# Performance work log

Measured on AMD Instinct MI355X. Metric: run time of the kernel, lower is better.

## Reference

```python
import jax, jax.numpy as jnp
import numpy as np

B, V, N, C = 32, 5, 196, 768
H = 768          # hidden_dim of score MLP
NUM_ITERS = 3


def setup_inputs() -> dict:
    key = jax.random.key(0)
    ks = jax.random.split(key, 6)
    scale = 1.0 / np.sqrt(C)
    x = jax.random.normal(ks[0], (B, V, N, C), dtype=jnp.float32)
    # per-view projection weights, stacked: [V, C, C] (no bias)
    w_views = jax.random.uniform(ks[1], (V, C, C), dtype=jnp.float32, minval=-scale, maxval=scale)
    # score MLP: Linear(2C -> H), Tanh, Linear(H -> 1)
    s1 = 1.0 / np.sqrt(2 * C)
    w1 = jax.random.uniform(ks[2], (2 * C, H), dtype=jnp.float32, minval=-s1, maxval=s1)
    b1 = jax.random.uniform(ks[3], (H,), dtype=jnp.float32, minval=-s1, maxval=s1)
    s2 = 1.0 / np.sqrt(H)
    w2 = jax.random.uniform(ks[4], (H, 1), dtype=jnp.float32, minval=-s2, maxval=s2)
    b2 = jax.random.uniform(ks[5], (1,), dtype=jnp.float32, minval=-s2, maxval=s2)
    return {"x": x, "w_views": w_views, "w1": w1, "b1": b1, "w2": w2, "b2": b2}


def reference(x, w_views, w1, b1, w2, b2):
    # x: [B, V, N, C]
    c = x.mean(axis=1)                                   # [B, N, C]
    # per-view projections are independent of c: compute once (same math)
    proj_x = jnp.einsum('bvnc,vcd->bvnd', x, w_views)    # [B, V, N, C]
    a = None
    for _ in range(NUM_ITERS):
        c_exp = jnp.broadcast_to(c[:, None], x.shape)    # [B, V, N, C]
        si = jnp.concatenate([x, c_exp], axis=-1)        # [B, V, N, 2C]
        h = jnp.tanh(jnp.einsum('bvnk,kh->bvnh', si, w1) + b1)
        s = (jnp.einsum('bvnh,ho->bvno', h, w2) + b2)[..., 0]  # [B, V, N]
        a = jax.nn.softmax(s, axis=1)                    # softmax over views
        c = jnp.einsum('bvn,bvnc->bnc', a, proj_x)       # weighted sum over V
    eps = 1e-8
    entropy = -(a * jnp.log(a + eps)).sum(axis=1)        # [B, N]
    r = 1.0 - entropy / np.log(V)
    return c, r
```

## Files before the change

kernel.cpp:

```cpp
#include <hip/hip_runtime.h>

#define CDIM   768
#define NSEQ   196
#define NVIEW  5
#define BN_TOT 6272
#define SLAB   4816896
#define WSLAB  589824

typedef __attribute__((ext_vector_type(8))) short short8;
typedef __attribute__((ext_vector_type(4))) float f32x4;

__device__ __forceinline__ float bf_lo(unsigned u) { return __uint_as_float(u << 16); }
__device__ __forceinline__ float bf_hi(unsigned u) { return __uint_as_float(u & 0xffff0000u); }
__device__ __forceinline__ unsigned short f2bf(float f) {
  unsigned u = __float_as_uint(f);
  return (unsigned short)((u + 0x7fffu + ((u >> 16) & 1u)) >> 16);
}
__device__ __forceinline__ unsigned pack2(float f0, float f1) {
  return (unsigned)f2bf(f0) | ((unsigned)f2bf(f1) << 16);
}
__device__ __forceinline__ float ftanh(float x) {
  x = fminf(fmaxf(x, -10.f), 10.f);
  float e = __expf(2.f * x);
  return (e - 1.f) / (e + 1.f);
}
__device__ __forceinline__ void async_cp16(const void* g, void* l) {
  __builtin_amdgcn_global_load_lds((const __attribute__((address_space(1))) unsigned*)g,
                                   (__attribute__((address_space(3))) unsigned*)l, 16, 0, 0);
}

__global__ __launch_bounds__(256) void k_tr2(const float* __restrict__ wv,
                                             const float* __restrict__ w1,
                                             const float* __restrict__ x,
                                             unsigned short* __restrict__ wvT,
                                             unsigned short* __restrict__ w1aT,
                                             unsigned short* __restrict__ w1bT,
                                             unsigned short* __restrict__ wvB,
                                             unsigned short* __restrict__ cb) {
  const int m = blockIdx.z;
  const int tx = threadIdx.x, ty = threadIdx.y, t = ty * 32 + tx;
  if (m == 7) {
    const int bidx = blockIdx.y * 24 + blockIdx.x;
    if (t < 192) {
      const int col = t * 4;
      for (int i = 0; i < 11; ++i) {
        const int bn = bidx * 11 + i;
        if (bn >= BN_TOT) break;
        const int b = bn / NSEQ, n = bn - b * NSEQ;
        const float* xp = x + ((size_t)(b * NVIEW) * NSEQ + n) * CDIM + col;
        float s0 = 0, s1 = 0, s2 = 0, s3 = 0;
#pragma unroll
        for (int v = 0; v < NVIEW; ++v) {
          float4 p = *(const float4*)(xp + (size_t)v * (NSEQ * CDIM));
          s0 += p.x; s1 += p.y; s2 += p.z; s3 += p.w;
        }
        uint2 o;
        o.x = pack2(s0 * 0.2f, s1 * 0.2f);
        o.y = pack2(s2 * 0.2f, s3 * 0.2f);
        *(uint2*)(cb + (size_t)bn * CDIM + col) = o;
      }
    }
    return;
  }
  __shared__ float tile[32][33];
  const float* src;
  unsigned short* dst;
  unsigned short* dstB = nullptr;
  if (m < NVIEW)      { src = wv + (size_t)m * WSLAB; dst = wvT + (size_t)m * WSLAB;
                        dstB = wvB + (size_t)m * WSLAB; }
  else if (m == NVIEW){ src = w1;                     dst = w1aT; }
  else                { src = w1 + WSLAB;             dst = w1bT; }
  const int x0 = blockIdx.x * 32, y0 = blockIdx.y * 32;
#pragma unroll
  for (int i = 0; i < 4; ++i) {
    float v = src[(size_t)(y0 + ty + i * 8) * CDIM + x0 + tx];
    tile[ty + i * 8][tx] = v;
    if (dstB) dstB[(size_t)(y0 + ty + i * 8) * CDIM + x0 + tx] = f2bf(v);
  }
  __syncthreads();
#pragma unroll
  for (int i = 0; i < 4; ++i)
    dst[(size_t)(x0 + ty + i * 8) * CDIM + y0 + tx] = f2bf(tile[tx][ty + i * 8]);
}

__global__ __launch_bounds__(256, 4) void k_pre(const unsigned short* __restrict__ w1bT,
                                                const unsigned short* __restrict__ wvB,
                                                const unsigned short* __restrict__ cb,
                                                unsigned short* __restrict__ wpT,
                                                unsigned short* __restrict__ cw1) {
  __shared__ __align__(16) unsigned short lds[16384];
  const int wk = blockIdx.x;
  const int t = threadIdx.x, w = t >> 6, lane = t & 63, lr = lane & 15, lq = lane >> 4;
  const int wm = (w >> 1) * 64, wn = (w & 1) * 64;
  const unsigned short *Abf, *Bt;
  unsigned short* C;
  int mrow0, colBase;
  if (wk < 180) {
    const int v = wk / 36, rem = wk % 36;
    mrow0 = (rem / 6) * 128; colBase = (rem % 6) * 128;
    Abf = w1bT; Bt = wvB + (size_t)v * WSLAB; C = wpT + (size_t)v * WSLAB;
  } else {
    const int j = wk - 180;
    mrow0 = (j / 6) * 128; colBase = (j % 6) * 128;
    Abf = cb; Bt = w1bT; C = cw1;
  }
  const int swz = ((t & 3) ^ ((t >> 3) & 3)) << 3;
  const unsigned short* gA = Abf + (size_t)(mrow0 + (t >> 2)) * CDIM + swz;
  const unsigned short* gB = Bt + (size_t)(colBase + (t >> 2)) * CDIM + swz;
  const int kch = ((lq ^ ((lr >> 1) & 3)) << 3);
#define CPA(kt, s) { unsigned short* d_ = lds + (s) * 8192 + (w << 9);                  \
    async_cp16(gA + (kt) * 32, d_);                                                     \
    async_cp16(gA + (kt) * 32 + (size_t)64 * CDIM, d_ + 2048); }
#define CPB(kt, s) { unsigned short* d_ = lds + (s) * 8192 + 4096 + (w << 9);           \
    async_cp16(gB + (kt) * 32, d_);                                                     \
    async_cp16(gB + (kt) * 32 + (size_t)64 * CDIM, d_ + 2048); }
  f32x4 acc[4][4] = {};
  CPA(0, 0); CPB(0, 0);
  asm volatile("s_waitcnt vmcnt(0)" ::: "memory");
  __builtin_amdgcn_s_barrier();
  for (int kt = 0; kt < 24; ++kt) {
    const int s = kt & 1;
    const unsigned short* bp = lds + s * 8192;
    if (kt < 23) { CPA(kt + 1, s ^ 1); CPB(kt + 1, s ^ 1); }
    short8 af[4], bf[4];
#pragma unroll
    for (int i = 0; i < 4; ++i) af[i] = *(const short8*)(bp + (wm + i * 16 + lr) * 32 + kch);
#pragma unroll
    for (int j = 0; j < 4; ++j) bf[j] = *(const short8*)(bp + 4096 + (wn + j * 16 + lr) * 32 + kch);
    __builtin_amdgcn_s_setprio(1);
#pragma unroll
    for (int i = 0; i < 4; ++i)
#pragma unroll
      for (int j = 0; j < 4; ++j)
        acc[i][j] = __builtin_amdgcn_mfma_f32_16x16x32_bf16(af[i], bf[j], acc[i][j], 0, 0, 0);
    __builtin_amdgcn_s_setprio(0);
    asm volatile("s_waitcnt vmcnt(0) lgkmcnt(0)" ::: "memory");
    __builtin_amdgcn_s_barrier();
  }
#undef CPA
#undef CPB
#pragma unroll
  for (int i = 0; i < 4; ++i)
#pragma unroll
    for (int j = 0; j < 4; ++j) {
      const int gr = mrow0 + wm + i * 16 + lq * 4;
      const int gc = colBase + wn + j * 16 + lr;
      unsigned short* cp = C + (size_t)gr * CDIM + gc;
#pragma unroll
      for (int r = 0; r < 4; ++r)
        cp[(size_t)r * CDIM] = f2bf(acc[i][j][r]);
    }
}

__global__ __launch_bounds__(256, 4) void gemm_m(const float* __restrict__ X,
                                                 const unsigned short* __restrict__ wvT,
                                                 const unsigned short* __restrict__ w1aT,
                                                 const unsigned short* __restrict__ wpT,
                                                 unsigned short* __restrict__ projb,
                                                 unsigned short* __restrict__ xw1b,
                                                 unsigned short* __restrict__ pw1b) {
  __shared__ __align__(16) unsigned short lds[16384];
  const int orig = blockIdx.x;
  const int xcd = orig & 7, slot0 = orig >> 3;
  const int wk = (xcd < 2 ? xcd * 552 : 1104 + (xcd - 2) * 551) + slot0;
  const int t = threadIdx.x, w = t >> 6, lane = t & 63, lr = lane & 15, lq = lane >> 4;
  const int wm = (w >> 1) * 64, wn = (w & 1) * 64;
  const int v = wk / 882, rem = wk % 882;
  const int mt = rem / 18, qq = rem % 18, sub = qq / 6;
  const int colBase = (qq % 6) * 128, mrow0 = mt * 128;
  const unsigned short* Bt = sub == 0 ? wvT + (size_t)v * WSLAB
                            : sub == 1 ? w1aT : wpT + (size_t)v * WSLAB;
  unsigned short* C = (sub == 0 ? projb : sub == 1 ? xw1b : pw1b) + (size_t)v * SLAB;
  const int r = mrow0 + (t >> 1), b = r / NSEQ, n = r - b * NSEQ;
  const float* aRow = X + ((size_t)((b * NVIEW + v) * NSEQ) + n) * CDIM + (t & 1) * 16;
  const int swz = ((t & 3) ^ ((t >> 3) & 3)) << 3;
  const unsigned short* gB = Bt + (size_t)(colBase + (t >> 2)) * CDIM + swz;
  const int sw = (t >> 2) & 3, c0 = (t & 1) * 2;
  const int wA0 = (t >> 1) * 32 + ((c0 ^ sw) << 3);
  const int wA1 = (t >> 1) * 32 + (((c0 + 1) ^ sw) << 3);
  const int kch = ((lq ^ ((lr >> 1) & 3)) << 3);
#define CPB(kt, s) { unsigned short* d_ = lds + (s) * 8192 + 4096 + (w << 9);           \
    async_cp16(gB + (kt) * 32, d_);                                                     \
    async_cp16(gB + (kt) * 32 + (size_t)64 * CDIM, d_ + 2048); }
#define LOADA(kt) { f0 = *(const float4*)(aRow + (kt) * 32);                            \
    f1 = *(const float4*)(aRow + (kt) * 32 + 4);                                        \
    f2 = *(const float4*)(aRow + (kt) * 32 + 8);                                        \
    f3 = *(const float4*)(aRow + (kt) * 32 + 12); }
#define PACKW(s) { uint4 u0, u1;                                                        \
    u0.x = pack2(f0.x, f0.y); u0.y = pack2(f0.z, f0.w);                                 \
    u0.z = pack2(f1.x, f1.y); u0.w = pack2(f1.z, f1.w);                                 \
    u1.x = pack2(f2.x, f2.y); u1.y = pack2(f2.z, f2.w);                                 \
    u1.z = pack2(f3.x, f3.y); u1.w = pack2(f3.z, f3.w);                                 \
    *(uint4*)(lds + (s) * 8192 + wA0) = u0;                                             \
    *(uint4*)(lds + (s) * 8192 + wA1) = u1; }
  f32x4 acc[4][4] = {};
  float4 f0, f1, f2, f3;
  LOADA(0); CPB(0, 0); PACKW(0);
  asm volatile("s_waitcnt vmcnt(0) lgkmcnt(0)" ::: "memory");
  __builtin_amdgcn_s_barrier();
  for (int kt = 0; kt < 24; ++kt) {
    const int s = kt & 1;
    const unsigned short* bp = lds + s * 8192;
    const bool pf = (kt < 23);
    if (pf) { LOADA(kt + 1); CPB(kt + 1, s ^ 1); }
    short8 af[4], bf[4];
#pragma unroll
    for (int i = 0; i < 4; ++i) af[i] = *(const short8*)(bp + (wm + i * 16 + lr) * 32 + kch);
#pragma unroll
    for (int j = 0; j < 4; ++j) bf[j] = *(const short8*)(bp + 4096 + (wn + j * 16 + lr) * 32 + kch);
    __builtin_amdgcn_s_setprio(1);
#pragma unroll
    for (int i = 0; i < 4; ++i)
#pragma unroll
      for (int j = 0; j < 4; ++j)
        acc[i][j] = __builtin_amdgcn_mfma_f32_16x16x32_bf16(af[i], bf[j], acc[i][j], 0, 0, 0);
    __builtin_amdgcn_s_setprio(0);
    if (pf) PACKW(s ^ 1);
    asm volatile("s_waitcnt vmcnt(0) lgkmcnt(0)" ::: "memory");
    __builtin_amdgcn_s_barrier();
  }
#undef CPB
#undef LOADA
#undef PACKW
#pragma unroll
  for (int i = 0; i < 4; ++i)
#pragma unroll
    for (int j = 0; j < 4; ++j) {
      const int gr = mrow0 + wm + i * 16 + lq * 4;
      const int gc = colBase + wn + j * 16 + lr;
      unsigned short* cp = C + (size_t)gr * CDIM + gc;
#pragma unroll
      for (int rr = 0; rr < 4; ++rr)
        cp[(size_t)rr * CDIM] = f2bf(acc[i][j][rr]);
    }
}

__global__ __launch_bounds__(192) void k_iter3(const unsigned short* __restrict__ xw1b,
                                               const unsigned short* __restrict__ cw1,
                                               const unsigned short* __restrict__ pw1b,
                                               const unsigned short* __restrict__ projb,
                                               const float* __restrict__ b1,
                                               const float* __restrict__ w2,
                                               float* __restrict__ outc,
                                               float* __restrict__ outr) {
  __shared__ float red[3][NVIEW];
  __shared__ float aa[NVIEW];
  const int bn = blockIdx.x, t = threadIdx.x, wid = t >> 6, lane = t & 63;
  const int h = t * 4;
  const float4 bv = *(const float4*)(b1 + h);
  const float4 wv = *(const float4*)(w2 + h);
  float cw[4];
  { uint2 c = *(const uint2*)(cw1 + (size_t)bn * CDIM + h);
    cw[0] = bf_lo(c.x); cw[1] = bf_hi(c.x); cw[2] = bf_lo(c.y); cw[3] = bf_hi(c.y); }
  float xw[NVIEW][4], pf[NVIEW][4];
#pragma unroll
  for (int v = 0; v < NVIEW; ++v) {
    uint2 q = *(const uint2*)(xw1b + ((size_t)v * BN_TOT + bn) * CDIM + h);
    xw[v][0] = bf_lo(q.x) + bv.x; xw[v][1] = bf_hi(q.x) + bv.y;
    xw[v][2] = bf_lo(q.y) + bv.z; xw[v][3] = bf_hi(q.y) + bv.w;
    uint2 p = *(const uint2*)(pw1b + ((size_t)v * BN_TOT + bn) * CDIM + h);
    pf[v][0] = bf_lo(p.x); pf[v][1] = bf_hi(p.x);
    pf[v][2] = bf_lo(p.y); pf[v][3] = bf_hi(p.y);
  }
  for (int it = 0; it < 3; ++it) {
    float part[NVIEW];
#pragma unroll
    for (int v = 0; v < NVIEW; ++v) {
      float p;
      p = wv.x * ftanh(xw[v][0] + cw[0]);
      p = fmaf(wv.y, ftanh(xw[v][1] + cw[1]), p);
      p = fmaf(wv.z, ftanh(xw[v][2] + cw[2]), p);
      p = fmaf(wv.w, ftanh(xw[v][3] + cw[3]), p);
      part[v] = p;
    }
#pragma unroll
    for (int off = 32; off > 0; off >>= 1)
#pragma unroll
      for (int v = 0; v < NVIEW; ++v) part[v] += __shfl_down(part[v], off);
    if (lane == 0)
#pragma unroll
      for (int v = 0; v < NVIEW; ++v) red[wid][v] = part[v];
    __syncthreads();
    if (t == 0) {
      float s[NVIEW];
#pragma unroll
      for (int v = 0; v < NVIEW; ++v) s[v] = red[0][v] + red[1][v] + red[2][v];
      float m = s[0];
#pragma unroll
      for (int v = 1; v < NVIEW; ++v) m = fmaxf(m, s[v]);
      float a[NVIEW], sum = 0.f;
#pragma unroll
      for (int v = 0; v < NVIEW; ++v) { a[v] = __expf(s[v] - m); sum += a[v]; }
      const float inv = 1.f / sum;
#pragma unroll
      for (int v = 0; v < NVIEW; ++v) { a[v] *= inv; aa[v] = a[v]; }
      if (it == 2) {
        float ent = 0.f;
#pragma unroll
        for (int v = 0; v < NVIEW; ++v) ent -= a[v] * logf(a[v] + 1e-8f);
        outr[bn] = 1.f - ent * 0.6213349345596119f;
      }
    }
    __syncthreads();
    if (it < 2) {
      float n0 = 0, n1 = 0, n2 = 0, n3 = 0;
#pragma unroll
      for (int v = 0; v < NVIEW; ++v) {
        const float av = aa[v];
        n0 = fmaf(av, pf[v][0], n0); n1 = fmaf(av, pf[v][1], n1);
        n2 = fmaf(av, pf[v][2], n2); n3 = fmaf(av, pf[v][3], n3);
      }
      cw[0] = n0; cw[1] = n1; cw[2] = n2; cw[3] = n3;
    } else {
      float r0 = 0, r1 = 0, r2 = 0, r3 = 0;
#pragma unroll
      for (int v = 0; v < NVIEW; ++v) {
        const float av = aa[v];
        uint2 p = *(const uint2*)(projb + ((size_t)v * BN_TOT + bn) * CDIM + h);
        r0 = fmaf(av, bf_lo(p.x), r0); r1 = fmaf(av, bf_hi(p.x), r1);
        r2 = fmaf(av, bf_lo(p.y), r2); r3 = fmaf(av, bf_hi(p.y), r3);
      }
      float4 of; of.x = r0; of.y = r1; of.z = r2; of.w = r3;
      *(float4*)(outc + (size_t)bn * CDIM + h) = of;
    }
  }
}

extern "C" void kernel_launch(void* const* d_in, const int* in_sizes, int n_in,
                              void* d_out, int out_size, void* d_ws, size_t ws_size,
                              hipStream_t stream) {
  (void)in_sizes; (void)n_in; (void)out_size; (void)ws_size;
  const float* x  = (const float*)d_in[0];
  const float* wv = (const float*)d_in[1];
  const float* w1 = (const float*)d_in[2];
  const float* b1 = (const float*)d_in[3];
  const float* w2 = (const float*)d_in[4];

  unsigned short* ws   = (unsigned short*)d_ws;
  unsigned short* wvT  = ws;
  unsigned short* w1aT = ws + 2949120;
  unsigned short* w1bT = ws + 3538944;
  unsigned short* projb= ws + 4128768;
  unsigned short* xw1b = ws + 28213248;
  unsigned short* wvB  = ws + 28213248;
  unsigned short* pw1b = ws + 52297728;
  unsigned short* cb   = ws + 76382208;
  unsigned short* cw1  = ws + 81199104;

  float* outc = (float*)d_out;
  float* outr = outc + SLAB;
  unsigned short* wpT  = (unsigned short*)d_out;

  k_tr2<<<dim3(24, 24, 8), dim3(32, 8), 0, stream>>>(wv, w1, x, wvT, w1aT, w1bT, wvB, cb);
  k_pre<<<474, 256, 0, stream>>>(w1bT, wvB, cb, wpT, cw1);
  gemm_m<<<4410, 256, 0, stream>>>(x, wvT, w1aT, wpT, projb, xw1b, pw1b);
  k_iter3<<<BN_TOT, 192, 0, stream>>>(xw1b, cw1, pw1b, projb, b1, w2, outc, outr);
}
```

Before: 436.3 us.

## Widen main GEMM tiles to 128x256 with 512 threads and fold c·W1b GEMM in

Replaces the 128x128, 256-thread main GEMM with a 128x256 tile using 8 waves, so each converted A tile of x is reused across twice as many output columns. It also moves the cb×W1b product out of k_pre and into the main GEMM grid as extra z-slices, shortening k_pre to 180 blocks and removing its tail. The cost is more LDS per block (48 KB double buffered) and a possible loss of occupancy. A-loading now uses 8 floats per thread instead of 16.

New measurement: 413.0 us. -5.3%, faster.

```diff
diff --git a/kernel.cpp b/kernel.cpp
--- a/kernel.cpp
+++ b/kernel.cpp
@@ -85,25 +85,16 @@
 
 __global__ __launch_bounds__(256, 4) void k_pre(const unsigned short* __restrict__ w1bT,
                                                 const unsigned short* __restrict__ wvB,
-                                                const unsigned short* __restrict__ cb,
-                                                unsigned short* __restrict__ wpT,
-                                                unsigned short* __restrict__ cw1) {
+                                                unsigned short* __restrict__ wpT) {
   __shared__ __align__(16) unsigned short lds[16384];
   const int wk = blockIdx.x;
   const int t = threadIdx.x, w = t >> 6, lane = t & 63, lr = lane & 15, lq = lane >> 4;
   const int wm = (w >> 1) * 64, wn = (w & 1) * 64;
-  const unsigned short *Abf, *Bt;
-  unsigned short* C;
-  int mrow0, colBase;
-  if (wk < 180) {
-    const int v = wk / 36, rem = wk % 36;
-    mrow0 = (rem / 6) * 128; colBase = (rem % 6) * 128;
-    Abf = w1bT; Bt = wvB + (size_t)v * WSLAB; C = wpT + (size_t)v * WSLAB;
-  } else {
-    const int j = wk - 180;
-    mrow0 = (j / 6) * 128; colBase = (j % 6) * 128;
-    Abf = cb; Bt = w1bT; C = cw1;
-  }
+  const int v = wk / 36, rem = wk % 36;
+  const int mrow0 = (rem / 6) * 128, colBase = (rem % 6) * 128;
+  const unsigned short* Abf = w1bT;
+  const unsigned short* Bt = wvB + (size_t)v * WSLAB;
+  unsigned short* C = wpT + (size_t)v * WSLAB;
   const int swz = ((t & 3) ^ ((t >> 3) & 3)) << 3;
   const unsigned short* gA = Abf + (size_t)(mrow0 + (t >> 2)) * CDIM + swz;
   const unsigned short* gB = Bt + (size_t)(colBase + (t >> 2)) * CDIM + swz;
@@ -152,57 +143,77 @@
     }
 }
 
-__global__ __launch_bounds__(256, 4) void gemm_m(const float* __restrict__ X,
-                                                 const unsigned short* __restrict__ wvT,
-                                                 const unsigned short* __restrict__ w1aT,
-                                                 const unsigned short* __restrict__ wpT,
-                                                 unsigned short* __restrict__ projb,
-                                                 unsigned short* __restrict__ xw1b,
-                                                 unsigned short* __restrict__ pw1b) {
-  __shared__ __align__(16) unsigned short lds[16384];
+__global__ __launch_bounds__(512, 4) void gemm_m16(const float* __restrict__ X,
+                                                   const unsigned short* __restrict__ wvT,
+                                                   const unsigned short* __restrict__ w1aT,
+                                                   const unsigned short* __restrict__ wpT,
+                                                   const unsigned short* __restrict__ w1bT,
+                                                   const unsigned short* __restrict__ cb,
+                                                   unsigned short* __restrict__ projb,
+                                                   unsigned short* __restrict__ xw1b,
+                                                   unsigned short* __restrict__ pw1b,
+                                                   unsigned short* __restrict__ cw1) {
+  __shared__ __align__(16) unsigned short lds[2 * 12288];
   const int orig = blockIdx.x;
-  const int xcd = orig & 7, slot0 = orig >> 3;
-  const int wk = (xcd < 2 ? xcd * 552 : 1104 + (xcd - 2) * 551) + slot0;
+  const int wk = (orig & 7) * 294 + (orig >> 3);
+  const int nt = wk % 3, mt = (wk / 3) % 49, z = wk / 147;
   const int t = threadIdx.x, w = t >> 6, lane = t & 63, lr = lane & 15, lq = lane >> 4;
-  const int wm = (w >> 1) * 64, wn = (w & 1) * 64;
-  const int v = wk / 882, rem = wk % 882;
-  const int mt = rem / 18, qq = rem % 18, sub = qq / 6;
-  const int colBase = (qq % 6) * 128, mrow0 = mt * 128;
-  const unsigned short* Bt = sub == 0 ? wvT + (size_t)v * WSLAB
-                            : sub == 1 ? w1aT : wpT + (size_t)v * WSLAB;
-  unsigned short* C = (sub == 0 ? projb : sub == 1 ? xw1b : pw1b) + (size_t)v * SLAB;
-  const int r = mrow0 + (t >> 1), b = r / NSEQ, n = r - b * NSEQ;
-  const float* aRow = X + ((size_t)((b * NVIEW + v) * NSEQ) + n) * CDIM + (t & 1) * 16;
+  const int wm = ((w >> 2) & 1) * 64;
+  const int wn = (w & 3) * 64;
+  const int colBase = nt * 256, mrow0 = mt * 128;
+
+  const bool zc = (z < 15);
+  const unsigned short* Bt;
+  unsigned short* C;
+  const float* aPtr = nullptr;
+  if (zc) {
+    const int v = z % 5, sub = z / 5;
+    Bt = (sub == 0) ? wvT + (size_t)v * WSLAB : (sub == 1) ? w1aT : wpT + (size_t)v * WSLAB;
+    C  = ((sub == 0) ? projb : (sub == 1) ? xw1b : pw1b) + (size_t)v * SLAB;
+    const int r = mrow0 + (t >> 2);
+    const int b = r / NSEQ, n = r - b * NSEQ;
+    aPtr = X + (size_t)((b * NVIEW + v) * NSEQ + n) * CDIM + (t & 3) * 8;
+  } else {
+    Bt = w1bT; C = cw1;
+  }
+
   const int swz = ((t & 3) ^ ((t >> 3) & 3)) << 3;
   const unsigned short* gB = Bt + (size_t)(colBase + (t >> 2)) * CDIM + swz;
-  const int sw = (t >> 2) & 3, c0 = (t & 1) * 2;
-  const int wA0 = (t >> 1) * 32 + ((c0 ^ sw) << 3);
-  const int wA1 = (t >> 1) * 32 + (((c0 + 1) ^ sw) << 3);
+  const unsigned short* gAb = zc ? nullptr
+                                 : cb + (size_t)(mrow0 + (t >> 2)) * CDIM + swz;
+  const int aswz = swz;
   const int kch = ((lq ^ ((lr >> 1) & 3)) << 3);
-#define CPB(kt, s) { unsigned short* d_ = lds + (s) * 8192 + 4096 + (w << 9);           \
-    async_cp16(gB + (kt) * 32, d_);                                                     \
-    async_cp16(gB + (kt) * 32 + (size_t)64 * CDIM, d_ + 2048); }
-#define LOADA(kt) { f0 = *(const float4*)(aRow + (kt) * 32);                            \
-    f1 = *(const float4*)(aRow + (kt) * 32 + 4);                                        \
-    f2 = *(const float4*)(aRow + (kt) * 32 + 8);                                        \
-    f3 = *(const float4*)(aRow + (kt) * 32 + 12); }
-#define PACKW(s) { uint4 u0, u1;                                                        \
-    u0.x = pack2(f0.x, f0.y); u0.y = pack2(f0.z, f0.w);                                 \
-    u0.z = pack2(f1.x, f1.y); u0.w = pack2(f1.z, f1.w);                                 \
-    u1.x = pack2(f2.x, f2.y); u1.y = pack2(f2.z, f2.w);                                 \
-    u1.z = pack2(f3.x, f3.y); u1.w = pack2(f3.z, f3.w);                                 \
-    *(uint4*)(lds + (s) * 8192 + wA0) = u0;                                             \
-    *(uint4*)(lds + (s) * 8192 + wA1) = u1; }
+
+#define STB(kt, s) { const unsigned short* sp_ = gB + (kt) * 32;                  \
+    unsigned short* dp_ = lds + (s) * 12288 + 4096 + (w << 9);                    \
+    async_cp16(sp_, dp_); async_cp16(sp_ + (size_t)128 * CDIM, dp_ + 4096); }
+#define STA1(kt, s) { async_cp16(gAb + (kt) * 32, lds + (s) * 12288 + (w << 9)); }
+#define STA0W(s) { uint4 qv_;                                                     \
+    qv_.x = pack2(pa0.x, pa0.y); qv_.y = pack2(pa0.z, pa0.w);                     \
+    qv_.z = pack2(pa1.x, pa1.y); qv_.w = pack2(pa1.z, pa1.w);                     \
+    *(uint4*)(lds + (s) * 12288 + (t >> 2) * 32 + aswz) = qv_; }
+
   f32x4 acc[4][4] = {};
-  float4 f0, f1, f2, f3;
-  LOADA(0); CPB(0, 0); PACKW(0);
+  float4 pa0{}, pa1{};
+
+  if (zc) { pa0 = *(const float4*)(aPtr); pa1 = *(const float4*)(aPtr + 4); }
+  else    { STA1(0, 0); }
+  STB(0, 0);
+  if (zc) STA0W(0);
   asm volatile("s_waitcnt vmcnt(0) lgkmcnt(0)" ::: "memory");
   __builtin_amdgcn_s_barrier();
+
   for (int kt = 0; kt < 24; ++kt) {
     const int s = kt & 1;
-    const unsigned short* bp = lds + s * 8192;
+    const unsigned short* bp = lds + s * 12288;
     const bool pf = (kt < 23);
-    if (pf) { LOADA(kt + 1); CPB(kt + 1, s ^ 1); }
+    if (pf) {
+      if (zc) {
+        pa0 = *(const float4*)(aPtr + (kt + 1) * 32);
+        pa1 = *(const float4*)(aPtr + (kt + 1) * 32 + 4);
+      } else { STA1(kt + 1, s ^ 1); }
+      STB(kt + 1, s ^ 1);
+    }
     short8 af[4], bf[4];
 #pragma unroll
     for (int i = 0; i < 4; ++i) af[i] = *(const short8*)(bp + (wm + i * 16 + lr) * 32 + kch);
@@ -215,13 +226,14 @@
       for (int j = 0; j < 4; ++j)
         acc[i][j] = __builtin_amdgcn_mfma_f32_16x16x32_bf16(af[i], bf[j], acc[i][j], 0, 0, 0);
     __builtin_amdgcn_s_setprio(0);
-    if (pf) PACKW(s ^ 1);
+    if (pf && zc) STA0W(s ^ 1);
     asm volatile("s_waitcnt vmcnt(0) lgkmcnt(0)" ::: "memory");
     __builtin_amdgcn_s_barrier();
   }
-#undef CPB
-#undef LOADA
-#undef PACKW
+#undef STB
+#undef STA1
+#undef STA0W
+
 #pragma unroll
   for (int i = 0; i < 4; ++i)
 #pragma unroll
@@ -230,8 +242,8 @@
       const int gc = colBase + wn + j * 16 + lr;
       unsigned short* cp = C + (size_t)gr * CDIM + gc;
 #pragma unroll
-      for (int rr = 0; rr < 4; ++rr)
-        cp[(size_t)rr * CDIM] = f2bf(acc[i][j][rr]);
+      for (int r = 0; r < 4; ++r)
+        cp[(size_t)r * CDIM] = f2bf(acc[i][j][r]);
     }
 }
 
@@ -352,7 +364,8 @@
   unsigned short* wpT  = (unsigned short*)d_out;
 
   k_tr2<<<dim3(24, 24, 8), dim3(32, 8), 0, stream>>>(wv, w1, x, wvT, w1aT, w1bT, wvB, cb);
-  k_pre<<<474, 256, 0, stream>>>(w1bT, wvB, cb, wpT, cw1);
-  gemm_m<<<4410, 256, 0, stream>>>(x, wvT, w1aT, wpT, projb, xw1b, pw1b);
+  k_pre<<<180, 256, 0, stream>>>(w1bT, wvB, wpT);
+  gemm_m16<<<2352, 512, 0, stream>>>(x, wvT, w1aT, wpT, w1bT, cb,
+                                     projb, xw1b, pw1b, cw1);
   k_iter3<<<BN_TOT, 192, 0, stream>>>(xw1b, cw1, pw1b, projb, b1, w2, outc, outr);
 }
```
